# Optimization experiments

Measured on AMD Instinct MI355X. Metric: run time of the kernel, lower is better.

Reference implementation:

```python
import jax, jax.numpy as jnp
import numpy as np

D_MODEL = 768
NUM_HEAD = 12
D_K = D_MODEL // NUM_HEAD
NEG_BIG = -1e9


def setup_inputs() -> dict:
    key = jax.random.key(0)
    ks = jax.random.split(key, 16)
    B, S, D = 16, 512, D_MODEL
    scale = 1.0 / np.sqrt(D)
    inp = {
        "q": jax.random.normal(ks[0], (B, S, D), jnp.float32),
        "k": jax.random.normal(ks[1], (B, S, D), jnp.float32),
        "v": jax.random.normal(ks[2], (B, S, D), jnp.float32),
        # padding mask: 1 where masked, broadcast over heads and query dim
        "mask": jax.random.randint(ks[3], (B, 1, 1, S), 0, 2).astype(jnp.float32),
        # adjacency bias broadcast over heads
        "adj": jax.random.uniform(ks[4], (B, 1, S, S), jnp.float32),
        "Wq": jax.random.normal(ks[5], (D, D), jnp.float32) * scale,
        "bq": jnp.zeros((D,), jnp.float32),
        "Wk": jax.random.normal(ks[6], (D, D), jnp.float32) * scale,
        "bk": jnp.zeros((D,), jnp.float32),
        "Wv": jax.random.normal(ks[7], (D, D), jnp.float32) * scale,
        "bv": jnp.zeros((D,), jnp.float32),
        "Wo": jax.random.normal(ks[8], (D, D), jnp.float32) * scale,
        "bo": jnp.zeros((D,), jnp.float32),
    }
    return inp


def reference(q, k, v, mask, adj, Wq, bq, Wk, bk, Wv, bv, Wo, bo):
    B, S, D = q.shape
    H, dk = NUM_HEAD, D_K

    def proj(x, W, b):
        # nn.Linear: x @ W.T + b, then split heads -> [B, H, S, dk]
        y = jnp.einsum('bsd,ed->bse', x, W) + b
        return y.reshape(B, S, H, dk).transpose(0, 2, 1, 3)

    qh = proj(q, Wq, bq)
    kh = proj(k, Wk, bk)
    vh = proj(v, Wv, bv)

    scores = jnp.einsum('bhqd,bhkd->bhqk', qh, kh) / jnp.sqrt(jnp.float32(dk))
    scores = scores + mask * NEG_BIG + adj  # broadcast over heads
    attn = jax.nn.softmax(scores, axis=-1)
    x = jnp.einsum('bhqk,bhkd->bhqd', attn, vh)
    x = x.transpose(0, 2, 1, 3).reshape(B, S, D)
    return jnp.einsum('bsd,ed->bse', x, Wo) + bo
```

## Files before the change

### kernel.cpp

```cpp
#include <hip/hip_runtime.h>
#include <hip/hip_bf16.h>

#define SEQ 512
#define DM 768
#define NH 12
#define DK 64
#define NB 16
#define WN (DM * DM)
#define HE ((size_t)NB * SEQ * DM)
#define BSS ((size_t)NB * SEQ * SEQ)

typedef __attribute__((ext_vector_type(8))) _Float16 f16x8;
typedef __attribute__((ext_vector_type(4))) float f32x4;

static __device__ __forceinline__ void gload16(const void* g, void* lds) {
    __builtin_amdgcn_global_load_lds(
        (const __attribute__((address_space(1))) unsigned int*)g,
        (__attribute__((address_space(3))) unsigned int*)lds, 16, 0, 0);
}

__global__ __launch_bounds__(256) void convert_wa(
    const float* __restrict__ Wq, const float* __restrict__ Wk,
    const float* __restrict__ Wv, const float* __restrict__ Wo,
    const float* __restrict__ adj, const float* __restrict__ mask,
    _Float16* __restrict__ dst, _Float16* __restrict__ adjm)
{
    const size_t W4 = 4u * WN;
    size_t i8 = ((size_t)blockIdx.x * 256 + threadIdx.x) * 8;
    f16x8 h;
    if (i8 < W4) {
        unsigned int s = (unsigned int)(i8 / WN);
        const float* src = s == 0 ? Wq : s == 1 ? Wk : s == 2 ? Wv : Wo;
        size_t off = i8 - (size_t)s * WN;
        float4 a = *(const float4*)(src + off);
        float4 b = *(const float4*)(src + off + 4);
        h[0] = (_Float16)a.x; h[1] = (_Float16)a.y; h[2] = (_Float16)a.z; h[3] = (_Float16)a.w;
        h[4] = (_Float16)b.x; h[5] = (_Float16)b.y; h[6] = (_Float16)b.z; h[7] = (_Float16)b.w;
        *(f16x8*)(dst + i8) = h;
    } else {
        size_t j = i8 - W4;
        int b = (int)(j >> 18);
        int col = (int)(j & (SEQ - 1));
        float4 a0 = *(const float4*)(adj + j);
        float4 a1 = *(const float4*)(adj + j + 4);
        const float* mp = mask + ((size_t)b << 9) + col;
        float4 m0 = *(const float4*)(mp);
        float4 m1 = *(const float4*)(mp + 4);
        h[0] = (_Float16)(a0.x - 30000.0f * m0.x);
        h[1] = (_Float16)(a0.y - 30000.0f * m0.y);
        h[2] = (_Float16)(a0.z - 30000.0f * m0.z);
        h[3] = (_Float16)(a0.w - 30000.0f * m0.w);
        h[4] = (_Float16)(a1.x - 30000.0f * m1.x);
        h[5] = (_Float16)(a1.y - 30000.0f * m1.y);
        h[6] = (_Float16)(a1.z - 30000.0f * m1.z);
        h[7] = (_Float16)(a1.w - 30000.0f * m1.w);
        *(f16x8*)(adjm + j) = h;
    }
}

__global__ __launch_bounds__(256) void proj_qkv(
    const float* __restrict__ Aq, const float* __restrict__ Ak,
    const float* __restrict__ Av, const _Float16* __restrict__ Wh,
    const float* __restrict__ bq, const float* __restrict__ bk, const float* __restrict__ bv,
    _Float16* __restrict__ P1, _Float16* __restrict__ P2, _Float16* __restrict__ P3)
{
    __shared__ _Float16 As[128][32];
    __shared__ _Float16 Bs[128][32];
    const int f = blockIdx.x;
    const int lg = (f & 7) * 144 + (f >> 3);
    const int sel = lg / 384;
    const int rem = lg - sel * 384;
    const int bm = (rem / 6) * 128, bn = (rem % 6) * 128;
    const float* A = sel == 0 ? Aq : sel == 1 ? Ak : Av;
    const _Float16* W = Wh + (size_t)sel * WN;
    const float* bias = sel == 0 ? bq : sel == 1 ? bk : bv;
    _Float16* O = sel == 0 ? P1 : sel == 1 ? P2 : P3;

    const int t = threadIdx.x, lane = t & 63, w = t >> 6;
    const int wm = w >> 1, wn = w & 1, g = lane >> 4, r16 = lane & 15;
    const int lrow = lane >> 2, lcol = (lane & 3) * 8;

    f32x4 acc[4][4] = {};

    const float* ga0 = A + (size_t)(bm + w * 32 + lrow) * DM + lcol;
    const float* ga1 = ga0 + (size_t)16 * DM;
    const _Float16* gb0 = W + (size_t)(bn + w * 32 + lrow) * DM + lcol;
    const _Float16* gb1 = gb0 + (size_t)16 * DM;
    _Float16* la0 = &As[w * 32 + lrow][lcol];
    _Float16* la1 = &As[w * 32 + 16 + lrow][lcol];

    for (int kk = 0; kk < DM; kk += 32) {
        gload16(gb0 + kk, &Bs[w * 32][0]);
        gload16(gb1 + kk, &Bs[w * 32 + 16][0]);
        {
            float4 a0 = *(const float4*)(ga0 + kk);
            float4 a1 = *(const float4*)(ga0 + kk + 4);
            float4 a2 = *(const float4*)(ga1 + kk);
            float4 a3 = *(const float4*)(ga1 + kk + 4);
            f16x8 h0, h1;
            h0[0] = (_Float16)a0.x; h0[1] = (_Float16)a0.y; h0[2] = (_Float16)a0.z; h0[3] = (_Float16)a0.w;
            h0[4] = (_Float16)a1.x; h0[5] = (_Float16)a1.y; h0[6] = (_Float16)a1.z; h0[7] = (_Float16)a1.w;
            h1[0] = (_Float16)a2.x; h1[1] = (_Float16)a2.y; h1[2] = (_Float16)a2.z; h1[3] = (_Float16)a2.w;
            h1[4] = (_Float16)a3.x; h1[5] = (_Float16)a3.y; h1[6] = (_Float16)a3.z; h1[7] = (_Float16)a3.w;
            *(f16x8*)la0 = h0;
            *(f16x8*)la1 = h1;
        }
        __syncthreads();
        f16x8 af[4], bf[4];
        #pragma unroll
        for (int mi = 0; mi < 4; ++mi)
            af[mi] = *(f16x8*)&As[wm * 64 + mi * 16 + r16][g * 8];
        #pragma unroll
        for (int ni = 0; ni < 4; ++ni)
            bf[ni] = *(f16x8*)&Bs[wn * 64 + ni * 16 + r16][g * 8];
        #pragma unroll
        for (int mi = 0; mi < 4; ++mi)
            #pragma unroll
            for (int ni = 0; ni < 4; ++ni)
                acc[mi][ni] = __builtin_amdgcn_mfma_f32_16x16x32_f16(af[mi], bf[ni], acc[mi][ni], 0, 0, 0);
        __syncthreads();
    }
    #pragma unroll
    for (int ni = 0; ni < 4; ++ni) {
        int n = bn + wn * 64 + ni * 16 + r16;
        float bv_ = bias[n];
        #pragma unroll
        for (int mi = 0; mi < 4; ++mi) {
            #pragma unroll
            for (int r = 0; r < 4; ++r) {
                int m = bm + wm * 64 + mi * 16 + g * 4 + r;
                O[(size_t)m * DM + n] = (_Float16)(acc[mi][ni][r] + bv_);
            }
        }
    }
}

__global__ __launch_bounds__(256) void proj_o(
    const _Float16* __restrict__ A, const _Float16* __restrict__ W,
    const float* __restrict__ bias, float* __restrict__ O32)
{
    __shared__ _Float16 As[128][32];
    __shared__ _Float16 Bs[128][32];
    const int f = blockIdx.x;
    const int lg = (f & 7) * 48 + (f >> 3);
    const int bm = (lg / 6) * 128, bn = (lg % 6) * 128;
    const int t = threadIdx.x, lane = t & 63, w = t >> 6;
    const int wm = w >> 1, wn = w & 1, g = lane >> 4, r16 = lane & 15;
    const int lrow = lane >> 2, lcol = (lane & 3) * 8;

    f32x4 acc[4][4] = {};

    const _Float16* ga0 = A + (size_t)(bm + w * 32 + lrow) * DM + lcol;
    const _Float16* ga1 = ga0 + (size_t)16 * DM;
    const _Float16* gb0 = W + (size_t)(bn + w * 32 + lrow) * DM + lcol;
    const _Float16* gb1 = gb0 + (size_t)16 * DM;

    for (int kk = 0; kk < DM; kk += 32) {
        gload16(ga0 + kk, &As[w * 32][0]);
        gload16(ga1 + kk, &As[w * 32 + 16][0]);
        gload16(gb0 + kk, &Bs[w * 32][0]);
        gload16(gb1 + kk, &Bs[w * 32 + 16][0]);
        __syncthreads();
        f16x8 af[4], bf[4];
        #pragma unroll
        for (int mi = 0; mi < 4; ++mi)
            af[mi] = *(f16x8*)&As[wm * 64 + mi * 16 + r16][g * 8];
        #pragma unroll
        for (int ni = 0; ni < 4; ++ni)
            bf[ni] = *(f16x8*)&Bs[wn * 64 + ni * 16 + r16][g * 8];
        #pragma unroll
        for (int mi = 0; mi < 4; ++mi)
            #pragma unroll
            for (int ni = 0; ni < 4; ++ni)
                acc[mi][ni] = __builtin_amdgcn_mfma_f32_16x16x32_f16(af[mi], bf[ni], acc[mi][ni], 0, 0, 0);
        __syncthreads();
    }
    #pragma unroll
    for (int ni = 0; ni < 4; ++ni) {
        int n = bn + wn * 64 + ni * 16 + r16;
        float bv_ = bias[n];
        #pragma unroll
        for (int mi = 0; mi < 4; ++mi) {
            #pragma unroll
            for (int r = 0; r < 4; ++r) {
                int m = bm + wm * 64 + mi * 16 + g * 4 + r;
                O32[(size_t)m * DM + n] = acc[mi][ni][r] + bv_;
            }
        }
    }
}

#define VSWI(d, kcol) ((d) * 72 + ((((kcol) * 2) ^ ((((d) >> 3) & 7) << 4)) >> 1))
__global__ __launch_bounds__(256) void attn(
    const _Float16* __restrict__ Qp, const _Float16* __restrict__ Kp,
    const _Float16* __restrict__ Vp, const _Float16* __restrict__ Adjm,
    _Float16* __restrict__ X)
{
    __shared__ _Float16 Ks[2][64 * 64];
    __shared__ _Float16 Vt[2][64 * 72];
    __shared__ _Float16 Ps[4][16][72];
    const int id = blockIdx.x;
    const int lid = (id & 7) * 192 + (id >> 3);
    const int h = lid % NH, qb = (lid / NH) & 7, b = lid / (NH * 8);
    const int t = threadIdx.x, lane = t & 63, w = t >> 6;
    const int g = lane >> 4, r16 = lane & 15;
    const int srow = t >> 2, sc = (t & 3) * 16;

    const _Float16* Qg = Qp + (size_t)(b * SEQ + qb * 64 + w * 16 + r16) * DM + h * DK;
    const f16x8 qf0 = *(const f16x8*)(Qg + g * 8);
    const f16x8 qf1 = *(const f16x8*)(Qg + 32 + g * 8);

    const _Float16* Kbh   = Kp + (size_t)(b * SEQ) * DM + h * DK;
    const _Float16* Vbase = Vp + (size_t)(b * SEQ) * DM + h * DK + sc;
    const _Float16* Abase = Adjm + ((size_t)b << 18)
                                 + (size_t)(qb * 64 + w * 16 + g * 4) * SEQ + r16;

    uint4 vv[2];
    _Float16 am[16];

#define STAGEK(KB, BUF) { _Pragma("unroll") for (int j_ = 0; j_ < 2; ++j_) { \
        const _Float16* src_ = Kbh + (size_t)((KB) * 64 + w * 16 + j_ * 8 + (lane >> 3)) * DM \
                              + (((lane & 7) ^ (lane >> 3)) * 8); \
        gload16(src_, &Ks[BUF][(w * 16 + j_ * 8) * 64]); } }
#define LOADV(KB) { const _Float16* vp_ = Vbase + (size_t)((KB) * 64 + srow) * DM; \
        vv[0] = ((const uint4*)vp_)[0]; vv[1] = ((const uint4*)vp_)[1]; }
#define LOADA(KB) { _Pragma("unroll") for (int r = 0; r < 4; ++r) \
        _Pragma("unroll") for (int cb = 0; cb < 4; ++cb) \
            am[r * 4 + cb] = Abase[(size_t)r * SEQ + (KB) * 64 + cb * 16]; }

    STAGEK(0, 0);
    __builtin_amdgcn_sched_barrier(0);
    LOADV(0);
    LOADA(0);

    float l_lane[4] = {0.f, 0.f, 0.f, 0.f};
    f32x4 o[4] = {};

    #pragma unroll
    for (int kb = 0; kb < 8; ++kb) {
        const int buf = kb & 1;
        {
            union { uint4 u[2]; _Float16 hh[16]; } cv;
            cv.u[0] = vv[0]; cv.u[1] = vv[1];
            _Float16* vt = &Vt[buf][0];
            #pragma unroll
            for (int i = 0; i < 16; ++i) vt[VSWI(sc + i, srow)] = cv.hh[i];
        }
        asm volatile("s_waitcnt lgkmcnt(0)" ::: "memory");
        __builtin_amdgcn_sched_barrier(0);
        __builtin_amdgcn_s_barrier();
        __builtin_amdgcn_sched_barrier(0);

        f32x4 sf[4] = {};
        __builtin_amdgcn_s_setprio(1);
        #pragma unroll
        for (int cb = 0; cb < 4; ++cb) {
            const int R = cb * 16 + r16;
            f16x8 k0 = *(f16x8*)&Ks[buf][R * 64 + ((g ^ (r16 & 7)) * 8)];
            f16x8 k1 = *(f16x8*)&Ks[buf][R * 64 + (((4 + g) ^ (r16 & 7)) * 8)];
            sf[cb] = __builtin_amdgcn_mfma_f32_16x16x32_f16(qf0, k0, sf[cb], 0, 0, 0);
            sf[cb] = __builtin_amdgcn_mfma_f32_16x16x32_f16(qf1, k1, sf[cb], 0, 0, 0);
        }
        __builtin_amdgcn_s_setprio(0);
        if (kb < 7) {
            STAGEK(kb + 1, buf ^ 1);
            __builtin_amdgcn_sched_barrier(0);
            LOADV(kb + 1);
        }
        #pragma unroll
        for (int cb = 0; cb < 4; ++cb)
            #pragma unroll
            for (int r = 0; r < 4; ++r) {
                float e = exp2f(fmaf(sf[cb][r], 0.18033688f,
                            fmaf((float)am[r * 4 + cb], 1.44269504f, -11.54156036f)));
                sf[cb][r] = e;
                l_lane[r] += e;
            }
        if (kb < 7) LOADA(kb + 1);
        #pragma unroll
        for (int cb = 0; cb < 4; ++cb)
            #pragma unroll
            for (int r = 0; r < 4; ++r)
                Ps[w][g * 4 + r][cb * 16 + r16] = (_Float16)sf[cb][r];
        __builtin_amdgcn_s_setprio(1);
        #pragma unroll
        for (int ks = 0; ks < 2; ++ks) {
            f16x8 pf = *(f16x8*)&Ps[w][r16][ks * 32 + g * 8];
            #pragma unroll
            for (int db = 0; db < 4; ++db) {
                f16x8 vf = *(f16x8*)&Vt[buf][VSWI(db * 16 + r16, ks * 32 + g * 8)];
                o[db] = __builtin_amdgcn_mfma_f32_16x16x32_f16(pf, vf, o[db], 0, 0, 0);
            }
        }
        __builtin_amdgcn_s_setprio(0);
    }
#undef STAGEK
#undef LOADV
#undef LOADA
    #pragma unroll
    for (int d = 1; d < 16; d <<= 1)
        #pragma unroll
        for (int r = 0; r < 4; ++r)
            l_lane[r] += __shfl_xor(l_lane[r], d);
    const int qrow = qb * 64 + w * 16 + g * 4;
    #pragma unroll
    for (int r = 0; r < 4; ++r) {
        float inv = 1.f / l_lane[r];
        _Float16* xp = X + (size_t)(b * SEQ + qrow + r) * DM + h * DK;
        #pragma unroll
        for (int db = 0; db < 4; ++db)
            xp[db * 16 + r16] = (_Float16)(o[db][r] * inv);
    }
}

extern "C" void kernel_launch(void* const* d_in, const int* in_sizes, int n_in,
                              void* d_out, int out_size, void* d_ws, size_t ws_size,
                              hipStream_t stream)
{
    const float* q    = (const float*)d_in[0];
    const float* k    = (const float*)d_in[1];
    const float* v    = (const float*)d_in[2];
    const float* mask = (const float*)d_in[3];
    const float* adj  = (const float*)d_in[4];
    const float* Wq   = (const float*)d_in[5];
    const float* bq   = (const float*)d_in[6];
    const float* Wk   = (const float*)d_in[7];
    const float* bk   = (const float*)d_in[8];
    const float* Wv   = (const float*)d_in[9];
    const float* bv   = (const float*)d_in[10];
    const float* Wo   = (const float*)d_in[11];
    const float* bo   = (const float*)d_in[12];
    float* out = (float*)d_out;

    _Float16* Wh = (_Float16*)d_ws;
    _Float16* P1 = Wh + 4 * WN;
    _Float16* P2 = P1 + HE;
    _Float16* P3 = P2 + HE;
    _Float16* AD = P3 + HE;
    _Float16* X  = AD + BSS;

    convert_wa<<<dim3(3200), dim3(256), 0, stream>>>(Wq, Wk, Wv, Wo, adj, mask, Wh, AD);
    proj_qkv<<<dim3(1152), dim3(256), 0, stream>>>(q, k, v, Wh, bq, bk, bv, P1, P2, P3);
    attn<<<dim3(1536), dim3(256), 0, stream>>>(P1, P2, P3, AD, X);
    proj_o<<<dim3(384), dim3(256), 0, stream>>>(X, Wh + 3 * WN, bo, out);
}
```

Before: 126.7 us.

## Double-buffer LDS and software-pipeline the QKV projection GEMM main loop

Adds two-stage LDS buffers to the fused QKV projection kernel and restructures the K loop into a prologue, steady state and epilogue. Global-to-LDS loads of the weight tile and register prefetch of the next fp32 activation tile overlap the MFMA compute on the current buffer, with one barrier per iteration instead of two. Explicit waitcnt and sched_barrier calls enforce the ordering. This doubles LDS use and raises register pressure, and correctness now depends on the hand-counted vmcnt values.

```diff
diff --git a/kernel.cpp b/kernel.cpp
--- a/kernel.cpp
+++ b/kernel.cpp
@@ -64,8 +64,8 @@
     const float* __restrict__ bq, const float* __restrict__ bk, const float* __restrict__ bv,
     _Float16* __restrict__ P1, _Float16* __restrict__ P2, _Float16* __restrict__ P3)
 {
-    __shared__ _Float16 As[128][32];
-    __shared__ _Float16 Bs[128][32];
+    __shared__ _Float16 As[2][128][32];
+    __shared__ _Float16 Bs[2][128][32];
     const int f = blockIdx.x;
     const int lg = (f & 7) * 144 + (f >> 3);
     const int sel = lg / 384;
@@ -81,45 +81,74 @@
     const int lrow = lane >> 2, lcol = (lane & 3) * 8;
 
     f32x4 acc[4][4] = {};
+    float4 ar[4];
 
     const float* ga0 = A + (size_t)(bm + w * 32 + lrow) * DM + lcol;
     const float* ga1 = ga0 + (size_t)16 * DM;
     const _Float16* gb0 = W + (size_t)(bn + w * 32 + lrow) * DM + lcol;
     const _Float16* gb1 = gb0 + (size_t)16 * DM;
-    _Float16* la0 = &As[w * 32 + lrow][lcol];
-    _Float16* la1 = &As[w * 32 + 16 + lrow][lcol];
-
-    for (int kk = 0; kk < DM; kk += 32) {
-        gload16(gb0 + kk, &Bs[w * 32][0]);
-        gload16(gb1 + kk, &Bs[w * 32 + 16][0]);
-        {
-            float4 a0 = *(const float4*)(ga0 + kk);
-            float4 a1 = *(const float4*)(ga0 + kk + 4);
-            float4 a2 = *(const float4*)(ga1 + kk);
-            float4 a3 = *(const float4*)(ga1 + kk + 4);
-            f16x8 h0, h1;
-            h0[0] = (_Float16)a0.x; h0[1] = (_Float16)a0.y; h0[2] = (_Float16)a0.z; h0[3] = (_Float16)a0.w;
-            h0[4] = (_Float16)a1.x; h0[5] = (_Float16)a1.y; h0[6] = (_Float16)a1.z; h0[7] = (_Float16)a1.w;
-            h1[0] = (_Float16)a2.x; h1[1] = (_Float16)a2.y; h1[2] = (_Float16)a2.z; h1[3] = (_Float16)a2.w;
-            h1[4] = (_Float16)a3.x; h1[5] = (_Float16)a3.y; h1[6] = (_Float16)a3.z; h1[7] = (_Float16)a3.w;
-            *(f16x8*)la0 = h0;
-            *(f16x8*)la1 = h1;
-        }
-        __syncthreads();
-        f16x8 af[4], bf[4];
-        #pragma unroll
-        for (int mi = 0; mi < 4; ++mi)
-            af[mi] = *(f16x8*)&As[wm * 64 + mi * 16 + r16][g * 8];
-        #pragma unroll
-        for (int ni = 0; ni < 4; ++ni)
-            bf[ni] = *(f16x8*)&Bs[wn * 64 + ni * 16 + r16][g * 8];
-        #pragma unroll
-        for (int mi = 0; mi < 4; ++mi)
-            #pragma unroll
-            for (int ni = 0; ni < 4; ++ni)
-                acc[mi][ni] = __builtin_amdgcn_mfma_f32_16x16x32_f16(af[mi], bf[ni], acc[mi][ni], 0, 0, 0);
-        __syncthreads();
-    }
+
+#define LOADA(KK) { ar[0] = *(const float4*)(ga0 + (KK)); ar[1] = *(const float4*)(ga0 + (KK) + 4); \
+                    ar[2] = *(const float4*)(ga1 + (KK)); ar[3] = *(const float4*)(ga1 + (KK) + 4); }
+#define GB(KK, BUF) { gload16(gb0 + (KK), &Bs[BUF][w * 32][0]); \
+                      gload16(gb1 + (KK), &Bs[BUF][w * 32 + 16][0]); }
+#define CVTW(BUF) { f16x8 h0, h1; \
+        h0[0] = (_Float16)ar[0].x; h0[1] = (_Float16)ar[0].y; h0[2] = (_Float16)ar[0].z; h0[3] = (_Float16)ar[0].w; \
+        h0[4] = (_Float16)ar[1].x; h0[5] = (_Float16)ar[1].y; h0[6] = (_Float16)ar[1].z; h0[7] = (_Float16)ar[1].w; \
+        h1[0] = (_Float16)ar[2].x; h1[1] = (_Float16)ar[2].y; h1[2] = (_Float16)ar[2].z; h1[3] = (_Float16)ar[2].w; \
+        h1[4] = (_Float16)ar[3].x; h1[5] = (_Float16)ar[3].y; h1[6] = (_Float16)ar[3].z; h1[7] = (_Float16)ar[3].w; \
+        *(f16x8*)&As[BUF][w * 32 + lrow][lcol] = h0; \
+        *(f16x8*)&As[BUF][w * 32 + 16 + lrow][lcol] = h1; }
+#define COMPUTE(BUF) { f16x8 af[4], bf[4]; \
+        _Pragma("unroll") for (int mi = 0; mi < 4; ++mi) \
+            af[mi] = *(f16x8*)&As[BUF][wm * 64 + mi * 16 + r16][g * 8]; \
+        _Pragma("unroll") for (int ni = 0; ni < 4; ++ni) \
+            bf[ni] = *(f16x8*)&Bs[BUF][wn * 64 + ni * 16 + r16][g * 8]; \
+        _Pragma("unroll") for (int mi = 0; mi < 4; ++mi) \
+            _Pragma("unroll") for (int ni = 0; ni < 4; ++ni) \
+                acc[mi][ni] = __builtin_amdgcn_mfma_f32_16x16x32_f16(af[mi], bf[ni], acc[mi][ni], 0, 0, 0); }
+
+    LOADA(0);
+    GB(0, 0);
+    __builtin_amdgcn_sched_barrier(0);
+    CVTW(0);
+    LOADA(32);
+    __builtin_amdgcn_sched_barrier(0);
+    asm volatile("s_waitcnt vmcnt(4)" ::: "memory");
+    asm volatile("s_waitcnt lgkmcnt(0)" ::: "memory");
+    __builtin_amdgcn_s_barrier();
+    __builtin_amdgcn_sched_barrier(0);
+
+    #pragma unroll 2
+    for (int tt = 0; tt < 22; ++tt) {
+        const int buf = tt & 1;
+        GB((tt + 1) * 32, buf ^ 1);
+        __builtin_amdgcn_sched_barrier(0);
+        COMPUTE(buf);
+        CVTW(buf ^ 1);
+        LOADA((tt + 2) * 32);
+        __builtin_amdgcn_sched_barrier(0);
+        asm volatile("s_waitcnt vmcnt(4)" ::: "memory");
+        asm volatile("s_waitcnt lgkmcnt(0)" ::: "memory");
+        __builtin_amdgcn_s_barrier();
+        __builtin_amdgcn_sched_barrier(0);
+    }
+    GB(23 * 32, 1);
+    __builtin_amdgcn_sched_barrier(0);
+    COMPUTE(0);
+    CVTW(1);
+    __builtin_amdgcn_sched_barrier(0);
+    asm volatile("s_waitcnt vmcnt(0)" ::: "memory");
+    asm volatile("s_waitcnt lgkmcnt(0)" ::: "memory");
+    __builtin_amdgcn_s_barrier();
+    __builtin_amdgcn_sched_barrier(0);
+    COMPUTE(1);
+
+#undef LOADA
+#undef GB
+#undef CVTW
+#undef COMPUTE
+
     #pragma unroll
     for (int ni = 0; ni < 4; ++ni) {
         int n = bn + wn * 64 + ni * 16 + r16;
```

After: 133.2 us. 1.05x slower.
